# Performance work log

Hardware: AMD Instinct MI355X
Metric: run time of the kernel (lower is better)

The kernel has to match this reference:

```python
import jax, jax.numpy as jnp
import numpy as np

B, N, D, K, CF = 2, 4096, 128, 32, 16
EI = 2 * D + 1  # edge_input_dim = 257 (edge_feat=0, fourier_feat=0)


def setup_inputs() -> dict:
    key = jax.random.key(0)
    ks = jax.random.split(key, 10)
    rn = lambda k, shp, s=0.05: jax.random.normal(k, shp, jnp.float32) * s
    return {
        "h": rn(ks[0], (B, N, D), 1.0),
        "x": rn(ks[1], (B, N, 3), 1.0),
        "mask": jnp.ones((B, N), dtype=bool),
        # edge_mlp: Linear(EI, 2EI) -> SiLU -> Linear(2EI, CF) -> SiLU
        "We1": rn(ks[2], (EI, 2 * EI)), "be1": jnp.zeros((2 * EI,), jnp.float32),
        "We2": rn(ks[3], (2 * EI, CF)), "be2": jnp.zeros((CF,), jnp.float32),
        # coors_mlp: Linear(CF, 4CF) -> SiLU -> Linear(4CF, 1)
        "Wc1": rn(ks[4], (CF, 4 * CF)), "bc1": jnp.zeros((4 * CF,), jnp.float32),
        "Wc2": rn(ks[5], (4 * CF, 1)), "bc2": jnp.zeros((1,), jnp.float32),
        # node_mlp: Linear(D+CF, 2D) -> SiLU -> Linear(2D, D)
        "Wn1": rn(ks[6], (D + CF, 2 * D)), "bn1": jnp.zeros((2 * D,), jnp.float32),
        "Wn2": rn(ks[7], (2 * D, D)), "bn2": jnp.zeros((D,), jnp.float32),
    }


def _forward(h, x, mask, We1, be1, We2, be2, Wc1, bc1, Wc2, bc2, Wn1, bn1, Wn2, bn2):
    silu = jax.nn.silu
    b, n, d = h.shape
    # pairwise relative coordinates and squared distances
    rel = x[:, :, None, :] - x[:, None, :, :]            # [b, n, n, 3]
    dist = jnp.sum(rel * rel, axis=-1)                   # [b, n, n]
    # top-K nearest neighbors (smallest distance)
    _, idx = jax.lax.top_k(-dist, K)                     # [b, n, K]
    rel_k = jnp.take_along_axis(rel, idx[..., None], axis=2)   # [b, n, K, 3]
    dist_k = jnp.take_along_axis(dist, idx, axis=2)[..., None]  # [b, n, K, 1]
    bidx = jnp.arange(b)[:, None, None]
    feats_j = h[bidx, idx]                               # [b, n, K, d]
    feats_i = jnp.broadcast_to(h[:, :, None, :], (b, n, K, d))
    edge_in = jnp.concatenate([feats_i, feats_j, dist_k], axis=-1)  # [b, n, K, 2d+1]
    # edge MLP
    m_ij = silu(silu(edge_in @ We1 + be1) @ We2 + be2)   # [b, n, K, CF]
    # coordinate weights
    cw = (silu(m_ij @ Wc1 + bc1) @ Wc2 + bc2)[..., 0]    # [b, n, K]
    mask_ij = mask[:, :, None] & mask[bidx, idx]         # [b, n, K]
    cw = jnp.where(mask_ij, cw, 0.0)
    coors_out = jnp.einsum('bij,bijc->bic', cw, rel_k) + x
    # node update
    m_i = m_ij.sum(axis=-2)                              # [b, n, CF]
    node_in = jnp.concatenate([h, m_i], axis=-1)
    node_out = silu(node_in @ Wn1 + bn1) @ Wn2 + bn2 + h
    return node_out, coors_out


def reference(h, x, mask, We1, be1, We2, be2, Wc1, bc1, Wc2, bc2, Wn1, bn1, Wn2, bn2):
    return _forward(h, x, mask, We1, be1, We2, be2, Wc1, bc1, Wc2, bc2, Wn1, bn1, Wn2, bn2)
```

## Files before the change

### kernel.cpp

```cpp
#include <hip/hip_runtime.h>
#include <hip/hip_bf16.h>

#define BB    2
#define NNODE 4096
#define DD    128
#define KK    32
#define CFX   16

typedef __attribute__((ext_vector_type(8))) short bf16x8;
typedef __attribute__((ext_vector_type(4))) float f32x4;

__device__ __forceinline__ unsigned short f2bf(float f) {
    __hip_bfloat16 h = __float2bfloat16(f);
    return *reinterpret_cast<unsigned short*>(&h);
}
__device__ __forceinline__ unsigned pk2(float lo, float hi) {
    __hip_bfloat162 v = __float22bfloat162_rn(make_float2(lo, hi));
    return *reinterpret_cast<unsigned*>(&v);
}
__device__ __forceinline__ float silu_f(float v) {
    float e = __expf(-v);
    return v * __builtin_amdgcn_rcpf(1.f + e);
}
__device__ __forceinline__ float dist3(float xi0, float xi1, float xi2,
                                       const float* __restrict__ xb, int j) {
    float d0 = __fsub_rn(xi0, xb[3 * j]);
    float d1 = __fsub_rn(xi1, xb[3 * j + 1]);
    float d2 = __fsub_rn(xi2, xb[3 * j + 2]);
    return __fadd_rn(__fadd_rn(__fmul_rn(d0, d0), __fmul_rn(d1, d1)), __fmul_rn(d2, d2));
}

__global__ void prep_kernel(const float* __restrict__ We1, const float* __restrict__ We2,
                            const float* __restrict__ Wn1, const float* __restrict__ Wn2,
                            unsigned short* __restrict__ W1pack, unsigned short* __restrict__ W2p2,
                            unsigned short* __restrict__ Wn1p, unsigned short* __restrict__ Wn2p) {
    int tid = blockIdx.x * 256 + threadIdx.x;
    int stride = gridDim.x * 256;
    for (int p = tid; p < 9 * 36 * 64 * 8; p += stride) {
        int i = p & 7, lane = (p >> 3) & 63, rest = p >> 9;
        int nb = rest % 36, ks = rest / 36;
        int n = nb * 16 + (lane & 15);
        int k = ks * 32 + 8 * (lane >> 4) + i;
        W1pack[p] = (k < 257 && n < 514) ? f2bf(We1[k * 514 + n]) : (unsigned short)0;
    }
    for (int p = tid; p < 4 * 5 * 64 * 8; p += stride) {
        int i = p & 7, lane = (p >> 3) & 63, rest = p >> 9;
        int ks2 = rest % 5, wn = rest / 5;
        int g = lane >> 4, f = lane & 15;
        int nloc = ks2 * 32 + 16 * (i >> 2) + 4 * g + (i & 3);
        int ng = wn * 144 + nloc;
        W2p2[p] = (nloc < 144 && ng < 514) ? f2bf(We2[ng * 16 + f]) : (unsigned short)0;
    }
    for (int p = tid; p < 5 * 16 * 64 * 8; p += stride) {
        int i = p & 7, lane = (p >> 3) & 63, rest = p >> 9;
        int nb = rest % 16, ks = rest / 16;
        int u = nb * 16 + (lane & 15);
        int k = ks * 32 + 8 * (lane >> 4) + i;
        Wn1p[p] = (k < 144) ? f2bf(Wn1[k * 256 + u]) : (unsigned short)0;
    }
    for (int p = tid; p < 8 * 8 * 64 * 8; p += stride) {
        int i = p & 7, lane = (p >> 3) & 63, rest = p >> 9;
        int nb = rest % 8, ks = rest / 8;
        int d = nb * 16 + (lane & 15);
        int k = ks * 32 + 8 * (lane >> 4) + i;
        Wn2p[p] = f2bf(Wn2[k * 128 + d]);
    }
}

#define EQCAP 36
#define CANDCAP 1024
__global__ __launch_bounds__(256) void knn_kernel(const float* __restrict__ x,
                                                  int* __restrict__ idx_o,
                                                  float* __restrict__ relk_o,
                                                  float* __restrict__ distk_o) {
    __shared__ unsigned hist[4][256];
    __shared__ unsigned wsum[4];
    __shared__ unsigned sel[2];
    __shared__ unsigned shA, shB;
    __shared__ int out_j[KK];
    __shared__ int eqbuf[EQCAP];
    __shared__ uint2 cand[CANDCAP];

    const int t = threadIdx.x;
    const int ln = t & 63, wv = t >> 6;
    const int gn = blockIdx.x;
    const int b = gn >> 12, i = gn & 4095;
    const float* xb = x + (size_t)b * NNODE * 3;
    const float xi0 = xb[3 * i], xi1 = xb[3 * i + 1], xi2 = xb[3 * i + 2];

    #pragma unroll
    for (int q2 = 0; q2 < 4; ++q2) hist[q2][t] = 0;
    __syncthreads();

    unsigned ub[16];
    #pragma unroll
    for (int s = 0; s < 16; ++s) {
        float d = dist3(xi0, xi1, xi2, xb, t + 256 * s);
        ub[s] = __float_as_uint(d);
        atomicAdd(&hist[wv][ub[s] >> 24], 1u);
    }
    __syncthreads();

    int kk = KK;
    {
        unsigned hv = hist[0][t] + hist[1][t] + hist[2][t] + hist[3][t];
        unsigned v = hv;
        #pragma unroll
        for (int off = 1; off < 64; off <<= 1) {
            unsigned o = __shfl_up(v, off, 64);
            if (ln >= off) v += o;
        }
        if (ln == 63) wsum[wv] = v;
        __syncthreads();
        unsigned add = 0;
        #pragma unroll
        for (int w = 0; w < 4; ++w) add += (w < wv) ? wsum[w] : 0u;
        unsigned incl = v + add, excl = incl - hv;
        if ((unsigned)kk > excl && (unsigned)kk <= incl) { sel[0] = (unsigned)t; sel[1] = (unsigned)kk - excl; }
        __syncthreads();
    }
    unsigned prefix = sel[0];
    kk = (int)sel[1];
    __syncthreads();

    unsigned pc = 0;
    #pragma unroll
    for (int s = 0; s < 16; ++s) {
        unsigned tb = ub[s] >> 24;
        pc += (tb < prefix) ? 0x10000u : (tb == prefix ? 1u : 0u);
    }
    {
        unsigned v = pc;
        #pragma unroll
        for (int off = 1; off < 64; off <<= 1) {
            unsigned o = __shfl_up(v, off, 64);
            if (ln >= off) v += o;
        }
        if (ln == 63) wsum[wv] = v;
        __syncthreads();
        unsigned add = 0;
        #pragma unroll
        for (int w = 0; w < 4; ++w) add += (w < wv) ? wsum[w] : 0u;
        unsigned incl = v + add, excl = incl - pc;
        if (t == 255) { shA = incl >> 16; shB = incl & 0xFFFFu; }
        __syncthreads();
        unsigned wl = excl >> 16, wc = excl & 0xFFFFu;
        #pragma unroll
        for (int s = 0; s < 16; ++s) {
            unsigned u = ub[s];
            unsigned tb = u >> 24;
            int j = t + 256 * s;
            if (tb < prefix) { out_j[wl++] = j; }
            else if (tb == prefix) { if (wc < CANDCAP) cand[wc] = make_uint2(u, (unsigned)j); ++wc; }
        }
    }
    __syncthreads();
    const unsigned totL0 = shA, totC = shB;
    const bool fullscan = (totC > CANDCAP);

    for (int r = 1; r < 4; ++r) {
        const int sh = 24 - 8 * r;
        #pragma unroll
        for (int q2 = 0; q2 < 4; ++q2) hist[q2][t] = 0;
        __syncthreads();
        if (!fullscan) {
            for (int ii = t; ii < (int)totC; ii += 256) {
                unsigned u = cand[ii].x;
                if ((u >> (sh + 8)) == prefix) atomicAdd(&hist[wv][(u >> sh) & 255], 1u);
            }
        } else {
            #pragma unroll
            for (int s = 0; s < 16; ++s) {
                unsigned u = ub[s];
                if ((u >> (sh + 8)) == prefix) atomicAdd(&hist[wv][(u >> sh) & 255], 1u);
            }
        }
        __syncthreads();
        unsigned hv = hist[0][t] + hist[1][t] + hist[2][t] + hist[3][t];
        unsigned v = hv;
        #pragma unroll
        for (int off = 1; off < 64; off <<= 1) {
            unsigned o = __shfl_up(v, off, 64);
            if (ln >= off) v += o;
        }
        if (ln == 63) wsum[wv] = v;
        __syncthreads();
        unsigned add = 0;
        #pragma unroll
        for (int w = 0; w < 4; ++w) add += (w < wv) ? wsum[w] : 0u;
        unsigned incl = v + add, excl = incl - hv;
        if ((unsigned)kk > excl && (unsigned)kk <= incl) { sel[0] = (unsigned)t; sel[1] = (unsigned)kk - excl; }
        __syncthreads();
        prefix = (prefix << 8) | sel[0];
        kk = (int)sel[1];
        __syncthreads();
    }
    const unsigned T = prefix;

    int totL;
    if (!fullscan) {
        unsigned pc2 = 0;
        for (int ii = t; ii < (int)totC; ii += 256) {
            unsigned u = cand[ii].x;
            pc2 += (u < T) ? 0x10000u : (u == T ? 1u : 0u);
        }
        unsigned v = pc2;
        #pragma unroll
        for (int off = 1; off < 64; off <<= 1) {
            unsigned o = __shfl_up(v, off, 64);
            if (ln >= off) v += o;
        }
        if (ln == 63) wsum[wv] = v;
        __syncthreads();
        unsigned add = 0;
        #pragma unroll
        for (int w = 0; w < 4; ++w) add += (w < wv) ? wsum[w] : 0u;
        unsigned incl = v + add, excl = incl - pc2;
        if (t == 255) { shA = incl >> 16; shB = incl & 0xFFFFu; }
        __syncthreads();
        unsigned w2 = totL0 + (excl >> 16), we = excl & 0xFFFFu;
        for (int ii = t; ii < (int)totC; ii += 256) {
            unsigned u = cand[ii].x;
            int j = (int)cand[ii].y;
            if (u < T) { out_j[w2++] = j; }
            else if (u == T) { if (we < EQCAP) eqbuf[we] = j; ++we; }
        }
        __syncthreads();
        totL = (int)(totL0 + shA);
        const unsigned totE = shB;
        if (t == 0) {
            int need = KK - totL;
            if (totE <= EQCAP) {
                for (int a = 1; a < (int)totE; ++a) {
                    int key = eqbuf[a], c = a - 1;
                    while (c >= 0 && eqbuf[c] > key) { eqbuf[c + 1] = eqbuf[c]; --c; }
                    eqbuf[c + 1] = key;
                }
                for (int q = 0; q < need; ++q) out_j[totL + q] = eqbuf[q];
            } else {
                int taken = 0;
                for (int j = 0; j < NNODE && taken < need; ++j)
                    if (__float_as_uint(dist3(xi0, xi1, xi2, xb, j)) == T) out_j[totL + taken++] = j;
            }
        }
    } else {
        unsigned pc2 = 0;
        #pragma unroll
        for (int s = 0; s < 16; ++s) {
            unsigned u = ub[s];
            pc2 += (u < T) ? 0x10000u : (u == T ? 1u : 0u);
        }
        unsigned v = pc2;
        #pragma unroll
        for (int off = 1; off < 64; off <<= 1) {
            unsigned o = __shfl_up(v, off, 64);
            if (ln >= off) v += o;
        }
        if (ln == 63) wsum[wv] = v;
        __syncthreads();
        unsigned add = 0;
        #pragma unroll
        for (int w = 0; w < 4; ++w) add += (w < wv) ? wsum[w] : 0u;
        unsigned incl = v + add, excl = incl - pc2;
        if (t == 255) { shA = incl >> 16; shB = incl & 0xFFFFu; }
        __syncthreads();
        unsigned w2 = excl >> 16, we = excl & 0xFFFFu;
        #pragma unroll
        for (int s = 0; s < 16; ++s) {
            unsigned u = ub[s];
            int j = t + 256 * s;
            if (u < T) { out_j[w2++] = j; }
            else if (u == T) { if (we < EQCAP) eqbuf[we] = j; ++we; }
        }
        __syncthreads();
        totL = (int)shA;
        const unsigned totE = shB;
        if (t == 0) {
            int need = KK - totL;
            if (totE <= EQCAP) {
                for (int a = 1; a < (int)totE; ++a) {
                    int key = eqbuf[a], c = a - 1;
                    while (c >= 0 && eqbuf[c] > key) { eqbuf[c + 1] = eqbuf[c]; --c; }
                    eqbuf[c + 1] = key;
                }
                for (int q = 0; q < need; ++q) out_j[totL + q] = eqbuf[q];
            } else {
                int taken = 0;
                for (int j = 0; j < NNODE && taken < need; ++j)
                    if (__float_as_uint(dist3(xi0, xi1, xi2, xb, j)) == T) out_j[totL + taken++] = j;
            }
        }
    }
    __syncthreads();

    if (t < KK) {
        int j = out_j[t];
        size_t eo = (size_t)gn * KK + t;
        idx_o[eo] = j;
        float r0 = __fsub_rn(xi0, xb[3 * j]);
        float r1 = __fsub_rn(xi1, xb[3 * j + 1]);
        float r2 = __fsub_rn(xi2, xb[3 * j + 2]);
        relk_o[eo * 3 + 0] = r0;
        relk_o[eo * 3 + 1] = r1;
        relk_o[eo * 3 + 2] = r2;
        distk_o[eo] = __fadd_rn(__fadd_rn(__fmul_rn(r0, r0), __fmul_rn(r1, r1)), __fmul_rn(r2, r2));
    }
}

__global__ __launch_bounds__(256, 2) void edge_kernel(
    const float* __restrict__ h, const float* __restrict__ x, const int* __restrict__ mask,
    const float* __restrict__ be1, const float* __restrict__ be2,
    const float* __restrict__ Wc1, const float* __restrict__ bc1,
    const float* __restrict__ Wc2, const float* __restrict__ bc2,
    const int* __restrict__ idx, const float* __restrict__ relk, const float* __restrict__ distk,
    const unsigned short* __restrict__ W1pack, const unsigned short* __restrict__ W2p2,
    float* __restrict__ m_i_out, float* __restrict__ coors_out)
{
    __shared__ unsigned short E2[64][168];
    __shared__ unsigned short hi_s[2][136];
    __shared__ float be1s[576];
    __shared__ int   j_s[64];
    __shared__ float cw_s[64];
    __shared__ float m_s4[4 * 64 * 16];
    __shared__ float m_sF[64 * 17];

    const int t = threadIdx.x;
    const int gn0 = blockIdx.x * 2;
    const int b = gn0 >> 12;
    const int wn = t >> 6, lane = t & 63;
    const int l15 = lane & 15, g = lane >> 4;

    if (t < 64) {
        size_t eo = (size_t)gn0 * KK + t;
        j_s[t] = idx[eo];
        float dv = distk[eo];
        ushort2* p = (ushort2*)&E2[t][128];
        p[0] = make_ushort2(f2bf(dv), 0);
        #pragma unroll
        for (int z = 1; z < 20; ++z) p[z] = make_ushort2(0, 0);
    }
    {
        int n = t >> 7, c = t & 127;
        hi_s[n][c] = f2bf(h[(size_t)(gn0 + n) * DD + c]);
    }
    for (int i2 = t; i2 < 576; i2 += 256) be1s[i2] = (i2 < 514) ? be1[i2] : 0.f;
    __syncthreads();

    for (int q = t; q < 64 * 32; q += 256) {
        int e = q >> 5, d4 = q & 31;
        int j = j_s[e];
        float4 v = *(const float4*)(h + ((size_t)b * NNODE + j) * DD + d4 * 4);
        *(uint2*)&E2[e][d4 * 4] = make_uint2(pk2(v.x, v.y), pk2(v.z, v.w));
    }
    __syncthreads();

    const bf16x8* W1v = (const bf16x8*)W1pack;
    const bf16x8* W2v = (const bf16x8*)W2p2;
    int erow[4];
    #pragma unroll
    for (int et = 0; et < 4; ++et) erow[et] = et * 16 + l15;

    f32x4 acc2[4];
    #pragma unroll
    for (int et = 0; et < 4; ++et)
        #pragma unroll
        for (int r = 0; r < 4; ++r) acc2[et][r] = 0.f;

    #pragma unroll
    for (int c = 0; c < 2; ++c) {
        f32x4 acc[4][4];
        #pragma unroll
        for (int nb = 0; nb < 4; ++nb)
            #pragma unroll
            for (int et = 0; et < 4; ++et)
                #pragma unroll
                for (int r = 0; r < 4; ++r) acc[nb][et][r] = 0.f;
        #pragma unroll
        for (int ks = 0; ks < 9; ++ks) {
            const bf16x8* wp = W1v + ((size_t)(ks * 36 + wn * 9 + c * 4)) * 64 + lane;
            bf16x8 afr[4];
            #pragma unroll
            for (int nb = 0; nb < 4; ++nb) afr[nb] = wp[nb * 64];
            bf16x8 bfr[4];
            if (ks < 4) {
                bf16x8 b0 = *(const bf16x8*)&hi_s[0][ks * 32 + 8 * g];
                bf16x8 b1 = *(const bf16x8*)&hi_s[1][ks * 32 + 8 * g];
                bfr[0] = b0; bfr[1] = b0; bfr[2] = b1; bfr[3] = b1;
            } else {
                #pragma unroll
                for (int et = 0; et < 4; ++et)
                    bfr[et] = *(const bf16x8*)&E2[erow[et]][(ks - 4) * 32 + 8 * g];
            }
            #pragma unroll
            for (int nb = 0; nb < 4; ++nb)
                #pragma unroll
                for (int et = 0; et < 4; ++et)
                    acc[nb][et] = __builtin_amdgcn_mfma_f32_16x16x32_bf16(afr[nb], bfr[et], acc[nb][et], 0, 0, 0);
        }
        #pragma unroll
        for (int nb = 0; nb < 4; ++nb) {
            f32x4 bv = *(const f32x4*)&be1s[wn * 144 + (c * 4 + nb) * 16 + 4 * g];
            #pragma unroll
            for (int et = 0; et < 4; ++et)
                #pragma unroll
                for (int r = 0; r < 4; ++r)
                    acc[nb][et][r] = silu_f(acc[nb][et][r] + bv[r]);
        }
        #pragma unroll
        for (int qq = 0; qq < 2; ++qq) {
            int ks2 = 2 * c + qq;
            bf16x8 a2 = W2v[(size_t)(wn * 5 + ks2) * 64 + lane];
            #pragma unroll
            for (int et = 0; et < 4; ++et) {
                union { unsigned u[4]; bf16x8 v; } cv;
                cv.u[0] = pk2(acc[2 * qq][et][0], acc[2 * qq][et][1]);
                cv.u[1] = pk2(acc[2 * qq][et][2], acc[2 * qq][et][3]);
                cv.u[2] = pk2(acc[2 * qq + 1][et][0], acc[2 * qq + 1][et][1]);
                cv.u[3] = pk2(acc[2 * qq + 1][et][2], acc[2 * qq + 1][et][3]);
                acc2[et] = __builtin_amdgcn_mfma_f32_16x16x32_bf16(a2, cv.v, acc2[et], 0, 0, 0);
            }
        }
    }
    {
        f32x4 acc8[4];
        #pragma unroll
        for (int et = 0; et < 4; ++et)
            #pragma unroll
            for (int r = 0; r < 4; ++r) acc8[et][r] = 0.f;
        #pragma unroll
        for (int ks = 0; ks < 9; ++ks) {
            bf16x8 af = W1v[((size_t)(ks * 36 + wn * 9 + 8)) * 64 + lane];
            bf16x8 bfr[4];
            if (ks < 4) {
                bf16x8 b0 = *(const bf16x8*)&hi_s[0][ks * 32 + 8 * g];
                bf16x8 b1 = *(const bf16x8*)&hi_s[1][ks * 32 + 8 * g];
                bfr[0] = b0; bfr[1] = b0; bfr[2] = b1; bfr[3] = b1;
            } else {
                #pragma unroll
                for (int et = 0; et < 4; ++et)
                    bfr[et] = *(const bf16x8*)&E2[erow[et]][(ks - 4) * 32 + 8 * g];
            }
            #pragma unroll
            for (int et = 0; et < 4; ++et)
                acc8[et] = __builtin_amdgcn_mfma_f32_16x16x32_bf16(af, bfr[et], acc8[et], 0, 0, 0);
        }
        f32x4 bv = *(const f32x4*)&be1s[wn * 144 + 128 + 4 * g];
        #pragma unroll
        for (int et = 0; et < 4; ++et)
            #pragma unroll
            for (int r = 0; r < 4; ++r)
                acc8[et][r] = silu_f(acc8[et][r] + bv[r]);
        bf16x8 a2 = W2v[(size_t)(wn * 5 + 4) * 64 + lane];
        #pragma unroll
        for (int et = 0; et < 4; ++et) {
            union { unsigned u[4]; bf16x8 v; } cv;
            cv.u[0] = pk2(acc8[et][0], acc8[et][1]);
            cv.u[1] = pk2(acc8[et][2], acc8[et][3]);
            cv.u[2] = 0; cv.u[3] = 0;
            acc2[et] = __builtin_amdgcn_mfma_f32_16x16x32_bf16(a2, cv.v, acc2[et], 0, 0, 0);
        }
    }
    #pragma unroll
    for (int et = 0; et < 4; ++et)
        *(f32x4*)&m_s4[((wn * 64) + erow[et]) * 16 + 4 * g] = acc2[et];
    __syncthreads();

    #pragma unroll
    for (int i2 = t; i2 < 64 * 16; i2 += 256) {
        int e = i2 >> 4, f = i2 & 15;
        float s = m_s4[e * 16 + f] + m_s4[(64 + e) * 16 + f]
                + m_s4[(128 + e) * 16 + f] + m_s4[(192 + e) * 16 + f];
        m_sF[e * 17 + f] = silu_f(s + be2[f]);
    }
    __syncthreads();

    {
        const int ee = t >> 2, q4 = t & 3;
        const int u0 = q4 * 16;
        float mm[16];
        #pragma unroll
        for (int f = 0; f < 16; ++f) mm[f] = m_sF[ee * 17 + f];
        float h2[16];
        {
            const float4* bp = (const float4*)(bc1 + u0);
            float4 b0 = bp[0], b1 = bp[1], b2v = bp[2], b3 = bp[3];
            h2[0]=b0.x; h2[1]=b0.y; h2[2]=b0.z; h2[3]=b0.w;
            h2[4]=b1.x; h2[5]=b1.y; h2[6]=b1.z; h2[7]=b1.w;
            h2[8]=b2v.x; h2[9]=b2v.y; h2[10]=b2v.z; h2[11]=b2v.w;
            h2[12]=b3.x; h2[13]=b3.y; h2[14]=b3.z; h2[15]=b3.w;
        }
        #pragma unroll
        for (int f = 0; f < 16; ++f) {
            const float4* wp = (const float4*)(Wc1 + (size_t)f * 64 + u0);
            float4 w0 = wp[0], w1 = wp[1], w2 = wp[2], w3 = wp[3];
            float v = mm[f];
            h2[0]  = fmaf(v, w0.x, h2[0]);  h2[1]  = fmaf(v, w0.y, h2[1]);
            h2[2]  = fmaf(v, w0.z, h2[2]);  h2[3]  = fmaf(v, w0.w, h2[3]);
            h2[4]  = fmaf(v, w1.x, h2[4]);  h2[5]  = fmaf(v, w1.y, h2[5]);
            h2[6]  = fmaf(v, w1.z, h2[6]);  h2[7]  = fmaf(v, w1.w, h2[7]);
            h2[8]  = fmaf(v, w2.x, h2[8]);  h2[9]  = fmaf(v, w2.y, h2[9]);
            h2[10] = fmaf(v, w2.z, h2[10]); h2[11] = fmaf(v, w2.w, h2[11]);
            h2[12] = fmaf(v, w3.x, h2[12]); h2[13] = fmaf(v, w3.y, h2[13]);
            h2[14] = fmaf(v, w3.z, h2[14]); h2[15] = fmaf(v, w3.w, h2[15]);
        }
        float cw = 0.f;
        const float4* cp = (const float4*)(Wc2 + u0);
        float4 c0 = cp[0], c1 = cp[1], c2 = cp[2], c3 = cp[3];
        const float wv[16] = {c0.x,c0.y,c0.z,c0.w, c1.x,c1.y,c1.z,c1.w,
                              c2.x,c2.y,c2.z,c2.w, c3.x,c3.y,c3.z,c3.w};
        #pragma unroll
        for (int r = 0; r < 16; ++r) cw = fmaf(silu_f(h2[r]), wv[r], cw);
        cw += __shfl_xor(cw, 1, 64);
        cw += __shfl_xor(cw, 2, 64);
        if (q4 == 0) {
            cw += bc2[0];
            int gnode = gn0 + (ee >> 5);
            int mi = mask[gnode];
            int mj = mask[b * NNODE + j_s[ee]];
            cw_s[ee] = (mi != 0 && mj != 0) ? cw : 0.f;
        }
    }
    __syncthreads();

    if (t < 32) {
        int n = t >> 4, f = t & 15;
        float s = 0.f;
        #pragma unroll
        for (int k2 = 0; k2 < 32; ++k2) s += m_sF[(n * 32 + k2) * 17 + f];
        m_i_out[(size_t)(gn0 + n) * CFX + f] = s;
    } else if (t < 38) {
        int r = t - 32;
        int n = r / 3, c = r - n * 3;
        const float* rp = relk + ((size_t)gn0 * KK + n * 32) * 3 + c;
        float s = 0.f;
        #pragma unroll
        for (int k2 = 0; k2 < 32; ++k2) s = fmaf(cw_s[n * 32 + k2], rp[k2 * 3], s);
        coors_out[(size_t)(gn0 + n) * 3 + c] = s + x[(size_t)(gn0 + n) * 3 + c];
    }
}

__global__ __launch_bounds__(256) void node_kernel(
    const float* __restrict__ h, const float* __restrict__ m_i,
    const unsigned short* __restrict__ Wn1p, const float* __restrict__ bn1,
    const unsigned short* __restrict__ Wn2p, const float* __restrict__ bn2,
    float* __restrict__ node_out)
{
    __shared__ unsigned short nin[32][168];
    __shared__ unsigned short hid[32][264];

    const int t = threadIdx.x;
    const int gn0 = blockIdx.x * 32;
    const int wn = t >> 6, lane = t & 63;
    const int l15 = lane & 15, g = lane >> 4;

    for (int q = t; q < 32 * 32; q += 256) {
        int node = q >> 5, c4 = q & 31;
        float4 v = *(const float4*)(h + (size_t)(gn0 + node) * DD + c4 * 4);
        *(uint2*)&nin[node][c4 * 4] = make_uint2(pk2(v.x, v.y), pk2(v.z, v.w));
    }
    if (t < 128) {
        int node = t >> 2, c4 = t & 3;
        float4 v = *(const float4*)(m_i + (size_t)(gn0 + node) * CFX + c4 * 4);
        *(uint2*)&nin[node][128 + c4 * 4] = make_uint2(pk2(v.x, v.y), pk2(v.z, v.w));
    } else if (t < 224) {
        int r = t - 128;
        int node = r / 3, cc = (r - node * 3) * 8;
        *(uint4*)&nin[node][144 + cc] = make_uint4(0, 0, 0, 0);
    }
    __syncthreads();
// ... 65 lines not shown
            float4 o;
            o.x = acc2[nb][et][0] + bv[0] + hv.x;
            o.y = acc2[nb][et][1] + bv[1] + hv.y;
            o.z = acc2[nb][et][2] + bv[2] + hv.z;
            o.w = acc2[nb][et][3] + bv[3] + hv.w;
            *(float4*)(node_out + (size_t)gnode * DD + d0) = o;
        }
    }
}

extern "C" void kernel_launch(void* const* d_in, const int* in_sizes, int n_in,
                              void* d_out, int out_size, void* d_ws, size_t ws_size,
                              hipStream_t stream) {
    const float* h   = (const float*)d_in[0];
    const float* x   = (const float*)d_in[1];
    const int*   mask= (const int*)d_in[2];
    const float* We1 = (const float*)d_in[3];
    const float* be1 = (const float*)d_in[4];
    const float* We2 = (const float*)d_in[5];
    const float* be2 = (const float*)d_in[6];
    const float* Wc1 = (const float*)d_in[7];
    const float* bc1 = (const float*)d_in[8];
    const float* Wc2 = (const float*)d_in[9];
    const float* bc2 = (const float*)d_in[10];
    const float* Wn1 = (const float*)d_in[11];
    const float* bn1 = (const float*)d_in[12];
    const float* Wn2 = (const float*)d_in[13];
    const float* bn2 = (const float*)d_in[14];

    float* node_out  = (float*)d_out;
    float* coors_out = node_out + (size_t)BB * NNODE * DD;

    char* ws = (char*)d_ws;
    int*   idx    = (int*)ws;            ws += (size_t)BB * NNODE * KK * 4;
    float* relk   = (float*)ws;          ws += (size_t)BB * NNODE * KK * 3 * 4;
    float* distk  = (float*)ws;          ws += (size_t)BB * NNODE * KK * 4;
    float* m_i    = (float*)ws;          ws += (size_t)BB * NNODE * CFX * 4;
    unsigned short* W1pack = (unsigned short*)ws;  ws += (size_t)9 * 36 * 64 * 8 * 2;
    unsigned short* W2p2   = (unsigned short*)ws;  ws += (size_t)4 * 5 * 64 * 8 * 2;
    unsigned short* Wn1p   = (unsigned short*)ws;  ws += (size_t)5 * 16 * 64 * 8 * 2;
    unsigned short* Wn2p   = (unsigned short*)ws;  ws += (size_t)8 * 8 * 64 * 8 * 2;

    prep_kernel<<<256, 256, 0, stream>>>(We1, We2, Wn1, Wn2, W1pack, W2p2, Wn1p, Wn2p);
    knn_kernel<<<BB * NNODE, 256, 0, stream>>>(x, idx, relk, distk);
    edge_kernel<<<BB * NNODE / 2, 256, 0, stream>>>(h, x, mask, be1, be2, Wc1, bc1, Wc2, bc2,
                                                    idx, relk, distk, W1pack, W2p2,
                                                    m_i, coors_out);
    node_kernel<<<BB * NNODE / 32, 256, 0, stream>>>(h, m_i, Wn1p, bn1, Wn2p, bn2, node_out);
}
```

Baseline: 328.7 us.

## Fuse kNN radix-select into edge kernel, removing idx/relk/dist global buffers

```diff
diff --git a/kernel.cpp b/kernel.cpp
--- a/kernel.cpp
+++ b/kernel.cpp
@@ -22,8 +22,8 @@
     float e = __expf(-v);
     return v * __builtin_amdgcn_rcpf(1.f + e);
 }
-__device__ __forceinline__ float dist3(float xi0, float xi1, float xi2,
-                                       const float* __restrict__ xb, int j) {
+__device__ __forceinline__ float dist3c(float xi0, float xi1, float xi2,
+                                        const float* __restrict__ xb, int j) {
     float d0 = __fsub_rn(xi0, xb[3 * j]);
     float d1 = __fsub_rn(xi1, xb[3 * j + 1]);
     float d2 = __fsub_rn(xi2, xb[3 * j + 2]);
@@ -69,250 +69,11 @@
 
 #define EQCAP 36
 #define CANDCAP 1024
-__global__ __launch_bounds__(256) void knn_kernel(const float* __restrict__ x,
-                                                  int* __restrict__ idx_o,
-                                                  float* __restrict__ relk_o,
-                                                  float* __restrict__ distk_o) {
-    __shared__ unsigned hist[4][256];
-    __shared__ unsigned wsum[4];
-    __shared__ unsigned sel[2];
-    __shared__ unsigned shA, shB;
-    __shared__ int out_j[KK];
-    __shared__ int eqbuf[EQCAP];
-    __shared__ uint2 cand[CANDCAP];
-
-    const int t = threadIdx.x;
-    const int ln = t & 63, wv = t >> 6;
-    const int gn = blockIdx.x;
-    const int b = gn >> 12, i = gn & 4095;
-    const float* xb = x + (size_t)b * NNODE * 3;
-    const float xi0 = xb[3 * i], xi1 = xb[3 * i + 1], xi2 = xb[3 * i + 2];
-
-    #pragma unroll
-    for (int q2 = 0; q2 < 4; ++q2) hist[q2][t] = 0;
-    __syncthreads();
-
-    unsigned ub[16];
-    #pragma unroll
-    for (int s = 0; s < 16; ++s) {
-        float d = dist3(xi0, xi1, xi2, xb, t + 256 * s);
-        ub[s] = __float_as_uint(d);
-        atomicAdd(&hist[wv][ub[s] >> 24], 1u);
-    }
-    __syncthreads();
-
-    int kk = KK;
-    {
-        unsigned hv = hist[0][t] + hist[1][t] + hist[2][t] + hist[3][t];
-        unsigned v = hv;
-        #pragma unroll
-        for (int off = 1; off < 64; off <<= 1) {
-            unsigned o = __shfl_up(v, off, 64);
-            if (ln >= off) v += o;
-        }
-        if (ln == 63) wsum[wv] = v;
-        __syncthreads();
-        unsigned add = 0;
-        #pragma unroll
-        for (int w = 0; w < 4; ++w) add += (w < wv) ? wsum[w] : 0u;
-        unsigned incl = v + add, excl = incl - hv;
-        if ((unsigned)kk > excl && (unsigned)kk <= incl) { sel[0] = (unsigned)t; sel[1] = (unsigned)kk - excl; }
-        __syncthreads();
-    }
-    unsigned prefix = sel[0];
-    kk = (int)sel[1];
-    __syncthreads();
-
-    unsigned pc = 0;
-    #pragma unroll
-    for (int s = 0; s < 16; ++s) {
-        unsigned tb = ub[s] >> 24;
-        pc += (tb < prefix) ? 0x10000u : (tb == prefix ? 1u : 0u);
-    }
-    {
-        unsigned v = pc;
-        #pragma unroll
-        for (int off = 1; off < 64; off <<= 1) {
-            unsigned o = __shfl_up(v, off, 64);
-            if (ln >= off) v += o;
-        }
-        if (ln == 63) wsum[wv] = v;
-        __syncthreads();
-        unsigned add = 0;
-        #pragma unroll
-        for (int w = 0; w < 4; ++w) add += (w < wv) ? wsum[w] : 0u;
-        unsigned incl = v + add, excl = incl - pc;
-        if (t == 255) { shA = incl >> 16; shB = incl & 0xFFFFu; }
-        __syncthreads();
-        unsigned wl = excl >> 16, wc = excl & 0xFFFFu;
-        #pragma unroll
-        for (int s = 0; s < 16; ++s) {
-            unsigned u = ub[s];
-            unsigned tb = u >> 24;
-            int j = t + 256 * s;
-            if (tb < prefix) { out_j[wl++] = j; }
-            else if (tb == prefix) { if (wc < CANDCAP) cand[wc] = make_uint2(u, (unsigned)j); ++wc; }
-        }
-    }
-    __syncthreads();
-    const unsigned totL0 = shA, totC = shB;
-    const bool fullscan = (totC > CANDCAP);
-
-    for (int r = 1; r < 4; ++r) {
-        const int sh = 24 - 8 * r;
-        #pragma unroll
-        for (int q2 = 0; q2 < 4; ++q2) hist[q2][t] = 0;
-        __syncthreads();
-        if (!fullscan) {
-            for (int ii = t; ii < (int)totC; ii += 256) {
-                unsigned u = cand[ii].x;
-                if ((u >> (sh + 8)) == prefix) atomicAdd(&hist[wv][(u >> sh) & 255], 1u);
-            }
-        } else {
-            #pragma unroll
-            for (int s = 0; s < 16; ++s) {
-                unsigned u = ub[s];
-                if ((u >> (sh + 8)) == prefix) atomicAdd(&hist[wv][(u >> sh) & 255], 1u);
-            }
-        }
-        __syncthreads();
-        unsigned hv = hist[0][t] + hist[1][t] + hist[2][t] + hist[3][t];
-        unsigned v = hv;
-        #pragma unroll
-        for (int off = 1; off < 64; off <<= 1) {
-            unsigned o = __shfl_up(v, off, 64);
-            if (ln >= off) v += o;
-        }
-        if (ln == 63) wsum[wv] = v;
-        __syncthreads();
-        unsigned add = 0;
-        #pragma unroll
-        for (int w = 0; w < 4; ++w) add += (w < wv) ? wsum[w] : 0u;
-        unsigned incl = v + add, excl = incl - hv;
-        if ((unsigned)kk > excl && (unsigned)kk <= incl) { sel[0] = (unsigned)t; sel[1] = (unsigned)kk - excl; }
-        __syncthreads();
-        prefix = (prefix << 8) | sel[0];
-        kk = (int)sel[1];
-        __syncthreads();
-    }
-    const unsigned T = prefix;
-
-    int totL;
-    if (!fullscan) {
-        unsigned pc2 = 0;
-        for (int ii = t; ii < (int)totC; ii += 256) {
-            unsigned u = cand[ii].x;
-            pc2 += (u < T) ? 0x10000u : (u == T ? 1u : 0u);
-        }
-        unsigned v = pc2;
-        #pragma unroll
-        for (int off = 1; off < 64; off <<= 1) {
-            unsigned o = __shfl_up(v, off, 64);
-            if (ln >= off) v += o;
-        }
-        if (ln == 63) wsum[wv] = v;
-        __syncthreads();
-        unsigned add = 0;
-        #pragma unroll
-        for (int w = 0; w < 4; ++w) add += (w < wv) ? wsum[w] : 0u;
-        unsigned incl = v + add, excl = incl - pc2;
-        if (t == 255) { shA = incl >> 16; shB = incl & 0xFFFFu; }
-        __syncthreads();
-        unsigned w2 = totL0 + (excl >> 16), we = excl & 0xFFFFu;
-        for (int ii = t; ii < (int)totC; ii += 256) {
-            unsigned u = cand[ii].x;
-            int j = (int)cand[ii].y;
-            if (u < T) { out_j[w2++] = j; }
-            else if (u == T) { if (we < EQCAP) eqbuf[we] = j; ++we; }
-        }
-        __syncthreads();
-        totL = (int)(totL0 + shA);
-        const unsigned totE = shB;
-        if (t == 0) {
-            int need = KK - totL;
-            if (totE <= EQCAP) {
-                for (int a = 1; a < (int)totE; ++a) {
-                    int key = eqbuf[a], c = a - 1;
-                    while (c >= 0 && eqbuf[c] > key) { eqbuf[c + 1] = eqbuf[c]; --c; }
-                    eqbuf[c + 1] = key;
-                }
-                for (int q = 0; q < need; ++q) out_j[totL + q] = eqbuf[q];
-            } else {
-                int taken = 0;
-                for (int j = 0; j < NNODE && taken < need; ++j)
-                    if (__float_as_uint(dist3(xi0, xi1, xi2, xb, j)) == T) out_j[totL + taken++] = j;
-            }
-        }
-    } else {
-        unsigned pc2 = 0;
-        #pragma unroll
-        for (int s = 0; s < 16; ++s) {
-            unsigned u = ub[s];
-            pc2 += (u < T) ? 0x10000u : (u == T ? 1u : 0u);
-        }
-        unsigned v = pc2;
-        #pragma unroll
-        for (int off = 1; off < 64; off <<= 1) {
-            unsigned o = __shfl_up(v, off, 64);
-            if (ln >= off) v += o;
-        }
-        if (ln == 63) wsum[wv] = v;
-        __syncthreads();
-        unsigned add = 0;
-        #pragma unroll
-        for (int w = 0; w < 4; ++w) add += (w < wv) ? wsum[w] : 0u;
-        unsigned incl = v + add, excl = incl - pc2;
-        if (t == 255) { shA = incl >> 16; shB = incl & 0xFFFFu; }
-        __syncthreads();
-        unsigned w2 = excl >> 16, we = excl & 0xFFFFu;
-        #pragma unroll
-        for (int s = 0; s < 16; ++s) {
-            unsigned u = ub[s];
-            int j = t + 256 * s;
-            if (u < T) { out_j[w2++] = j; }
-            else if (u == T) { if (we < EQCAP) eqbuf[we] = j; ++we; }
-        }
-        __syncthreads();
-        totL = (int)shA;
-        const unsigned totE = shB;
-        if (t == 0) {
-            int need = KK - totL;
-            if (totE <= EQCAP) {
-                for (int a = 1; a < (int)totE; ++a) {
-                    int key = eqbuf[a], c = a - 1;
-                    while (c >= 0 && eqbuf[c] > key) { eqbuf[c + 1] = eqbuf[c]; --c; }
-                    eqbuf[c + 1] = key;
-                }
-                for (int q = 0; q < need; ++q) out_j[totL + q] = eqbuf[q];
-            } else {
-                int taken = 0;
-                for (int j = 0; j < NNODE && taken < need; ++j)
-                    if (__float_as_uint(dist3(xi0, xi1, xi2, xb, j)) == T) out_j[totL + taken++] = j;
-            }
-        }
-    }
-    __syncthreads();
-
-    if (t < KK) {
-        int j = out_j[t];
-        size_t eo = (size_t)gn * KK + t;
-        idx_o[eo] = j;
-        float r0 = __fsub_rn(xi0, xb[3 * j]);
-        float r1 = __fsub_rn(xi1, xb[3 * j + 1]);
-        float r2 = __fsub_rn(xi2, xb[3 * j + 2]);
-        relk_o[eo * 3 + 0] = r0;
-        relk_o[eo * 3 + 1] = r1;
-        relk_o[eo * 3 + 2] = r2;
-        distk_o[eo] = __fadd_rn(__fadd_rn(__fmul_rn(r0, r0), __fmul_rn(r1, r1)), __fmul_rn(r2, r2));
-    }
-}
-
 __global__ __launch_bounds__(256, 2) void edge_kernel(
     const float* __restrict__ h, const float* __restrict__ x, const int* __restrict__ mask,
     const float* __restrict__ be1, const float* __restrict__ be2,
     const float* __restrict__ Wc1, const float* __restrict__ bc1,
     const float* __restrict__ Wc2, const float* __restrict__ bc2,
-    const int* __restrict__ idx, const float* __restrict__ relk, const float* __restrict__ distk,
     const unsigned short* __restrict__ W1pack, const unsigned short* __restrict__ W2p2,
     float* __restrict__ m_i_out, float* __restrict__ coors_out)
 {
@@ -323,29 +84,279 @@
     __shared__ float cw_s[64];
     __shared__ float m_s4[4 * 64 * 16];
     __shared__ float m_sF[64 * 17];
+    __shared__ float dist_e[64];
+    __shared__ float rel_s[64][3];
 
     const int t = threadIdx.x;
     const int gn0 = blockIdx.x * 2;
     const int b = gn0 >> 12;
     const int wn = t >> 6, lane = t & 63;
     const int l15 = lane & 15, g = lane >> 4;
-
-    if (t < 64) {
-        size_t eo = (size_t)gn0 * KK + t;
-        j_s[t] = idx[eo];
-        float dv = distk[eo];
-        ushort2* p = (ushort2*)&E2[t][128];
-        p[0] = make_ushort2(f2bf(dv), 0);
-        #pragma unroll
-        for (int z = 1; z < 20; ++z) p[z] = make_ushort2(0, 0);
-    }
+    const int ln = lane, wv = wn;
+
     {
         int n = t >> 7, c = t & 127;
         hi_s[n][c] = f2bf(h[(size_t)(gn0 + n) * DD + c]);
     }
     for (int i2 = t; i2 < 576; i2 += 256) be1s[i2] = (i2 < 514) ? be1[i2] : 0.f;
+
+    {
+        unsigned* histA = (unsigned*)m_s4;
+        uint2*    candA = (uint2*)(m_s4 + 2048);
+        unsigned* wsum  = (unsigned*)m_sF;
+        unsigned* sel   = wsum + 4;
+        unsigned* shAB  = sel + 2;
+        int* out_jA     = (int*)(shAB + 2);
+        int* eqbufA     = out_jA + 32;
+
+        const float* xb = x + (size_t)b * NNODE * 3;
+        const int i0 = gn0 & 4095;
+        float xi[2][3];
+        #pragma unroll
+        for (int q = 0; q < 2; ++q) {
+            xi[q][0] = xb[3 * (i0 + q)];
+            xi[q][1] = xb[3 * (i0 + q) + 1];
+            xi[q][2] = xb[3 * (i0 + q) + 2];
+        }
+        for (int z = t; z < 2048; z += 256) histA[z] = 0;
+        __syncthreads();
+
+        unsigned ub[2][16];
+        #pragma unroll
+        for (int s = 0; s < 16; ++s) {
+            int j = t + 256 * s;
+            float xj0 = xb[3 * j], xj1 = xb[3 * j + 1], xj2 = xb[3 * j + 2];
+            #pragma unroll
+            for (int q = 0; q < 2; ++q) {
+                float d0 = __fsub_rn(xi[q][0], xj0);
+                float d1 = __fsub_rn(xi[q][1], xj1);
+                float d2 = __fsub_rn(xi[q][2], xj2);
+                float d = __fadd_rn(__fadd_rn(__fmul_rn(d0, d0), __fmul_rn(d1, d1)), __fmul_rn(d2, d2));
+                ub[q][s] = __float_as_uint(d);
+                atomicAdd(&histA[(q * 4 + wv) * 256 + (ub[q][s] >> 24)], 1u);
+            }
+        }
+        __syncthreads();
+
+        #pragma unroll
+        for (int q = 0; q < 2; ++q) {
+            int kk = KK;
+            {
+                unsigned hv = histA[(q * 4 + 0) * 256 + t] + histA[(q * 4 + 1) * 256 + t]
+                            + histA[(q * 4 + 2) * 256 + t] + histA[(q * 4 + 3) * 256 + t];
+                unsigned v = hv;
+                #pragma unroll
+                for (int off = 1; off < 64; off <<= 1) {
+                    unsigned o = __shfl_up(v, off, 64);
+                    if (ln >= off) v += o;
+                }
+                if (ln == 63) wsum[wv] = v;
+                __syncthreads();
+                unsigned add = 0;
+                #pragma unroll
+                for (int w = 0; w < 4; ++w) add += (w < wv) ? wsum[w] : 0u;
+                unsigned incl = v + add, excl = incl - hv;
+                if ((unsigned)kk > excl && (unsigned)kk <= incl) { sel[0] = (unsigned)t; sel[1] = (unsigned)kk - excl; }
+                __syncthreads();
+            }
+            unsigned prefix = sel[0];
+            kk = (int)sel[1];
+            __syncthreads();
+
+            unsigned pc = 0;
+            #pragma unroll
+            for (int s = 0; s < 16; ++s) {
+                unsigned tb = ub[q][s] >> 24;
+                pc += (tb < prefix) ? 0x10000u : (tb == prefix ? 1u : 0u);
+            }
+            {
+                unsigned v = pc;
+                #pragma unroll
+                for (int off = 1; off < 64; off <<= 1) {
+                    unsigned o = __shfl_up(v, off, 64);
+                    if (ln >= off) v += o;
+                }
+                if (ln == 63) wsum[wv] = v;
+                __syncthreads();
+                unsigned add = 0;
+                #pragma unroll
+                for (int w = 0; w < 4; ++w) add += (w < wv) ? wsum[w] : 0u;
+                unsigned incl = v + add, excl = incl - pc;
+                if (t == 255) { shAB[0] = incl >> 16; shAB[1] = incl & 0xFFFFu; }
+                __syncthreads();
+                unsigned wl = excl >> 16, wc = excl & 0xFFFFu;
+                #pragma unroll
+                for (int s = 0; s < 16; ++s) {
+                    unsigned u = ub[q][s];
+                    unsigned tb = u >> 24;
+                    int j = t + 256 * s;
+                    if (tb < prefix) { out_jA[wl++] = j; }
+                    else if (tb == prefix) { if (wc < CANDCAP) candA[wc] = make_uint2(u, (unsigned)j); ++wc; }
+                }
+            }
+            __syncthreads();
+            const unsigned totL0 = shAB[0], totC = shAB[1];
+            const bool fullscan = (totC > CANDCAP);
+
+            for (int r = 1; r < 4; ++r) {
+                const int sh = 24 - 8 * r;
+                #pragma unroll
+                for (int q2 = 0; q2 < 4; ++q2) histA[q2 * 256 + t] = 0;
+                __syncthreads();
+                if (!fullscan) {
+                    for (int ii = t; ii < (int)totC; ii += 256) {
+                        unsigned u = candA[ii].x;
+                        if ((u >> (sh + 8)) == prefix) atomicAdd(&histA[wv * 256 + ((u >> sh) & 255)], 1u);
+                    }
+                } else {
+                    #pragma unroll
+                    for (int s = 0; s < 16; ++s) {
+                        unsigned u = ub[q][s];
+                        if ((u >> (sh + 8)) == prefix) atomicAdd(&histA[wv * 256 + ((u >> sh) & 255)], 1u);
+                    }
+                }
+                __syncthreads();
+                unsigned hv = histA[t] + histA[256 + t] + histA[512 + t] + histA[768 + t];
+                unsigned v = hv;
+                #pragma unroll
+                for (int off = 1; off < 64; off <<= 1) {
+                    unsigned o = __shfl_up(v, off, 64);
+                    if (ln >= off) v += o;
+                }
+                if (ln == 63) wsum[wv] = v;
+                __syncthreads();
+                unsigned add = 0;
+                #pragma unroll
+                for (int w = 0; w < 4; ++w) add += (w < wv) ? wsum[w] : 0u;
+                unsigned incl = v + add, excl = incl - hv;
+                if ((unsigned)kk > excl && (unsigned)kk <= incl) { sel[0] = (unsigned)t; sel[1] = (unsigned)kk - excl; }
+                __syncthreads();
+                prefix = (prefix << 8) | sel[0];
+                kk = (int)sel[1];
+                __syncthreads();
+            }
+            const unsigned T = prefix;
+
+            int totL;
+            if (!fullscan) {
+                unsigned pc2 = 0;
+                for (int ii = t; ii < (int)totC; ii += 256) {
+                    unsigned u = candA[ii].x;
+                    pc2 += (u < T) ? 0x10000u : (u == T ? 1u : 0u);
+                }
+                unsigned v = pc2;
+                #pragma unroll
+                for (int off = 1; off < 64; off <<= 1) {
+                    unsigned o = __shfl_up(v, off, 64);
+                    if (ln >= off) v += o;
+                }
+                if (ln == 63) wsum[wv] = v;
+                __syncthreads();
+                unsigned add = 0;
+                #pragma unroll
+                for (int w = 0; w < 4; ++w) add += (w < wv) ? wsum[w] : 0u;
+                unsigned incl = v + add, excl = incl - pc2;
+                if (t == 255) { shAB[0] = incl >> 16; shAB[1] = incl & 0xFFFFu; }
+                __syncthreads();
+                unsigned w2 = totL0 + (excl >> 16), we = excl & 0xFFFFu;
+                for (int ii = t; ii < (int)totC; ii += 256) {
+                    unsigned u = candA[ii].x;
+                    int j = (int)candA[ii].y;
+                    if (u < T) { out_jA[w2++] = j; }
+                    else if (u == T) { if (we < EQCAP) eqbufA[we] = j; ++we; }
+                }
+                __syncthreads();
+                totL = (int)(totL0 + shAB[0]);
+                const unsigned totE = shAB[1];
+                if (t == 0) {
+                    int need = KK - totL;
+                    if (totE <= EQCAP) {
+                        for (int a = 1; a < (int)totE; ++a) {
+                            int key = eqbufA[a], c = a - 1;
+                            while (c >= 0 && eqbufA[c] > key) { eqbufA[c + 1] = eqbufA[c]; --c; }
+                            eqbufA[c + 1] = key;
+                        }
+                        for (int q3 = 0; q3 < need; ++q3) out_jA[totL + q3] = eqbufA[q3];
+                    } else {
+                        int taken = 0;
+                        for (int j = 0; j < NNODE && taken < need; ++j)
+                            if (__float_as_uint(dist3c(xi[q][0], xi[q][1], xi[q][2], xb, j)) == T)
+                                out_jA[totL + taken++] = j;
+                    }
+                }
+            } else {
+                unsigned pc2 = 0;
+                #pragma unroll
+                for (int s = 0; s < 16; ++s) {
+                    unsigned u = ub[q][s];
+                    pc2 += (u < T) ? 0x10000u : (u == T ? 1u : 0u);
+                }
+                unsigned v = pc2;
+                #pragma unroll
+                for (int off = 1; off < 64; off <<= 1) {
+                    unsigned o = __shfl_up(v, off, 64);
+                    if (ln >= off) v += o;
+                }
+                if (ln == 63) wsum[wv] = v;
+                __syncthreads();
+                unsigned add = 0;
+                #pragma unroll
+                for (int w = 0; w < 4; ++w) add += (w < wv) ? wsum[w] : 0u;
+                unsigned incl = v + add, excl = incl - pc2;
+                if (t == 255) { shAB[0] = incl >> 16; shAB[1] = incl & 0xFFFFu; }
+                __syncthreads();
+                unsigned w2 = excl >> 16, we = excl & 0xFFFFu;
+                #pragma unroll
+                for (int s = 0; s < 16; ++s) {
+                    unsigned u = ub[q][s];
+                    int j = t + 256 * s;
+                    if (u < T) { out_jA[w2++] = j; }
+                    else if (u == T) { if (we < EQCAP) eqbufA[we] = j; ++we; }
+                }
+                __syncthreads();
+                totL = (int)shAB[0];
+                const unsigned totE = shAB[1];
+                if (t == 0) {
+                    int need = KK - totL;
+                    if (totE <= EQCAP) {
+                        for (int a = 1; a < (int)totE; ++a) {
+                            int key = eqbufA[a], c = a - 1;
+                            while (c >= 0 && eqbufA[c] > key) { eqbufA[c + 1] = eqbufA[c]; --c; }
+                            eqbufA[c + 1] = key;
+                        }
+                        for (int q3 = 0; q3 < need; ++q3) out_jA[totL + q3] = eqbufA[q3];
+                    } else {
+                        int taken = 0;
+                        for (int j = 0; j < NNODE && taken < need; ++j)
+                            if (__float_as_uint(dist3c(xi[q][0], xi[q][1], xi[q][2], xb, j)) == T)
+                                out_jA[totL + taken++] = j;
+                    }
+                }
+            }
+            __syncthreads();
+
+            if (t < KK) {
+                int j = out_jA[t];
+                int e = q * 32 + t;
+                j_s[e] = j;
+                float r0 = __fsub_rn(xi[q][0], xb[3 * j]);
+                float r1 = __fsub_rn(xi[q][1], xb[3 * j + 1]);
+                float r2 = __fsub_rn(xi[q][2], xb[3 * j + 2]);
+                rel_s[e][0] = r0;
+                rel_s[e][1] = r1;
+                rel_s[e][2] = r2;
+                dist_e[e] = __fadd_rn(__fadd_rn(__fmul_rn(r0, r0), __fmul_rn(r1, r1)), __fmul_rn(r2, r2));
+            }
+            __syncthreads();
+        }
+    }
+    if (t < 64) {
+        ushort2* p = (ushort2*)&E2[t][128];
+        p[0] = make_ushort2(f2bf(dist_e[t]), 0);
+        #pragma unroll
+        for (int z = 1; z < 20; ++z) p[z] = make_ushort2(0, 0);
+    }
     __syncthreads();
-
     for (int q = t; q < 64 * 32; q += 256) {
         int e = q >> 5, d4 = q & 31;
         int j = j_s[e];
@@ -506,10 +517,10 @@
         float cw = 0.f;
         const float4* cp = (const float4*)(Wc2 + u0);
         float4 c0 = cp[0], c1 = cp[1], c2 = cp[2], c3 = cp[3];
-        const float wv[16] = {c0.x,c0.y,c0.z,c0.w, c1.x,c1.y,c1.z,c1.w,
-                              c2.x,c2.y,c2.z,c2.w, c3.x,c3.y,c3.z,c3.w};
-        #pragma unroll
-        for (int r = 0; r < 16; ++r) cw = fmaf(silu_f(h2[r]), wv[r], cw);
+        const float wv2[16] = {c0.x,c0.y,c0.z,c0.w, c1.x,c1.y,c1.z,c1.w,
+                               c2.x,c2.y,c2.z,c2.w, c3.x,c3.y,c3.z,c3.w};
+        #pragma unroll
+        for (int r = 0; r < 16; ++r) cw = fmaf(silu_f(h2[r]), wv2[r], cw);
         cw += __shfl_xor(cw, 1, 64);
         cw += __shfl_xor(cw, 2, 64);
         if (q4 == 0) {
@@ -531,10 +542,9 @@
     } else if (t < 38) {
         int r = t - 32;
         int n = r / 3, c = r - n * 3;
-        const float* rp = relk + ((size_t)gn0 * KK + n * 32) * 3 + c;
         float s = 0.f;
         #pragma unroll
-        for (int k2 = 0; k2 < 32; ++k2) s = fmaf(cw_s[n * 32 + k2], rp[k2 * 3], s);
+        for (int k2 = 0; k2 < 32; ++k2) s = fmaf(cw_s[n * 32 + k2], rel_s[n * 32 + k2][c], s);
         coors_out[(size_t)(gn0 + n) * 3 + c] = s + x[(size_t)(gn0 + n) * 3 + c];
     }
 }
@@ -666,9 +676,6 @@
     float* coors_out = node_out + (size_t)BB * NNODE * DD;
 
     char* ws = (char*)d_ws;
-    int*   idx    = (int*)ws;            ws += (size_t)BB * NNODE * KK * 4;
-    float* relk   = (float*)ws;          ws += (size_t)BB * NNODE * KK * 3 * 4;
-    float* distk  = (float*)ws;          ws += (size_t)BB * NNODE * KK * 4;
     float* m_i    = (float*)ws;          ws += (size_t)BB * NNODE * CFX * 4;
     unsigned short* W1pack = (unsigned short*)ws;  ws += (size_t)9 * 36 * 64 * 8 * 2;
     unsigned short* W2p2   = (unsigned short*)ws;  ws += (size_t)4 * 5 * 64 * 8 * 2;
@@ -676,9 +683,7 @@
     unsigned short* Wn2p   = (unsigned short*)ws;  ws += (size_t)8 * 8 * 64 * 8 * 2;
 
     prep_kernel<<<256, 256, 0, stream>>>(We1, We2, Wn1, Wn2, W1pack, W2p2, Wn1p, Wn2p);
-    knn_kernel<<<BB * NNODE, 256, 0, stream>>>(x, idx, relk, distk);
     edge_kernel<<<BB * NNODE / 2, 256, 0, stream>>>(h, x, mask, be1, be2, Wc1, bc1, Wc2, bc2,
-                                                    idx, relk, distk, W1pack, W2p2,
-                                                    m_i, coors_out);
+                                                    W1pack, W2p2, m_i, coors_out);
     node_kernel<<<BB * NNODE / 32, 256, 0, stream>>>(h, m_i, Wn1p, bn1, Wn2p, bn2, node_out);
 }
```

After: 360.7 us. 1.1x slower.

## Precompute per-node h_i·We1 term once instead of per edge

Applied to the files above, without the earlier changes.

```diff
diff --git a/kernel.cpp b/kernel.cpp
--- a/kernel.cpp
+++ b/kernel.cpp
@@ -64,6 +64,51 @@
         int d = nb * 16 + (lane & 15);
         int k = ks * 32 + 8 * (lane >> 4) + i;
         Wn2p[p] = f2bf(Wn2[k * 128 + d]);
+    }
+}
+
+__global__ __launch_bounds__(256) void pre_kernel(
+    const float* __restrict__ h, const float* __restrict__ be1,
+    const unsigned short* __restrict__ W1pack, float* __restrict__ pre_g)
+{
+    __shared__ unsigned short nin[16][136];
+    const int t = threadIdx.x;
+    const int gn0 = blockIdx.x * 16;
+    const int wn = t >> 6, lane = t & 63;
+    const int l15 = lane & 15, g = lane >> 4;
+
+    for (int q = t; q < 16 * 32; q += 256) {
+        int node = q >> 5, c4 = q & 31;
+        float4 v = *(const float4*)(h + (size_t)(gn0 + node) * DD + c4 * 4);
+        *(uint2*)&nin[node][c4 * 4] = make_uint2(pk2(v.x, v.y), pk2(v.z, v.w));
+    }
+    __syncthreads();
+
+    const bf16x8* W1v = (const bf16x8*)W1pack;
+    f32x4 acc[9];
+    #pragma unroll
+    for (int nb = 0; nb < 9; ++nb)
+        #pragma unroll
+        for (int r = 0; r < 4; ++r) acc[nb][r] = 0.f;
+    #pragma unroll
+    for (int ks = 0; ks < 4; ++ks) {
+        bf16x8 bfr = *(const bf16x8*)&nin[l15][ks * 32 + 8 * g];
+        #pragma unroll
+        for (int nb = 0; nb < 9; ++nb) {
+            bf16x8 af = W1v[((size_t)(ks * 36 + wn * 9 + nb)) * 64 + lane];
+            acc[nb] = __builtin_amdgcn_mfma_f32_16x16x32_bf16(af, bfr, acc[nb], 0, 0, 0);
+        }
+    }
+    float* outp = pre_g + (size_t)(gn0 + l15) * 576;
+    #pragma unroll
+    for (int nb = 0; nb < 9; ++nb) {
+        int n0 = wn * 144 + nb * 16 + 4 * g;
+        float4 o;
+        o.x = acc[nb][0] + ((n0 + 0) < 514 ? be1[n0 + 0] : 0.f);
+        o.y = acc[nb][1] + ((n0 + 1) < 514 ? be1[n0 + 1] : 0.f);
+        o.z = acc[nb][2] + ((n0 + 2) < 514 ? be1[n0 + 2] : 0.f);
+        o.w = acc[nb][3] + ((n0 + 3) < 514 ? be1[n0 + 3] : 0.f);
+        *(float4*)(outp + n0) = o;
     }
 }
 
@@ -309,16 +354,16 @@
 
 __global__ __launch_bounds__(256, 2) void edge_kernel(
     const float* __restrict__ h, const float* __restrict__ x, const int* __restrict__ mask,
-    const float* __restrict__ be1, const float* __restrict__ be2,
+    const float* __restrict__ be2,
     const float* __restrict__ Wc1, const float* __restrict__ bc1,
     const float* __restrict__ Wc2, const float* __restrict__ bc2,
     const int* __restrict__ idx, const float* __restrict__ relk, const float* __restrict__ distk,
     const unsigned short* __restrict__ W1pack, const unsigned short* __restrict__ W2p2,
+    const float* __restrict__ pre_g,
     float* __restrict__ m_i_out, float* __restrict__ coors_out)
 {
     __shared__ unsigned short E2[64][168];
-    __shared__ unsigned short hi_s[2][136];
-    __shared__ float be1s[576];
+    __shared__ float pre_s[2 * 576];
     __shared__ int   j_s[64];
     __shared__ float cw_s[64];
     __shared__ float m_s4[4 * 64 * 16];
@@ -340,10 +385,10 @@
         for (int z = 1; z < 20; ++z) p[z] = make_ushort2(0, 0);
     }
     {
-        int n = t >> 7, c = t & 127;
-        hi_s[n][c] = f2bf(h[(size_t)(gn0 + n) * DD + c]);
-    }
-    for (int i2 = t; i2 < 576; i2 += 256) be1s[i2] = (i2 < 514) ? be1[i2] : 0.f;
+        const float4* src = (const float4*)(pre_g + (size_t)gn0 * 576);
+        float4* dst = (float4*)pre_s;
+        for (int i2 = t; i2 < 288; i2 += 256) dst[i2] = src[i2];
+    }
     __syncthreads();
 
     for (int q = t; q < 64 * 32; q += 256) {
@@ -373,24 +418,17 @@
         for (int nb = 0; nb < 4; ++nb)
             #pragma unroll
             for (int et = 0; et < 4; ++et)
-                #pragma unroll
-                for (int r = 0; r < 4; ++r) acc[nb][et][r] = 0.f;
-        #pragma unroll
-        for (int ks = 0; ks < 9; ++ks) {
-            const bf16x8* wp = W1v + ((size_t)(ks * 36 + wn * 9 + c * 4)) * 64 + lane;
+                acc[nb][et] = *(const f32x4*)&pre_s[(et >> 1) * 576 + wn * 144 + (c * 4 + nb) * 16 + 4 * g];
+        #pragma unroll
+        for (int ks = 0; ks < 5; ++ks) {
+            const bf16x8* wp = W1v + ((size_t)((ks + 4) * 36 + wn * 9 + c * 4)) * 64 + lane;
             bf16x8 afr[4];
             #pragma unroll
             for (int nb = 0; nb < 4; ++nb) afr[nb] = wp[nb * 64];
             bf16x8 bfr[4];
-            if (ks < 4) {
-                bf16x8 b0 = *(const bf16x8*)&hi_s[0][ks * 32 + 8 * g];
-                bf16x8 b1 = *(const bf16x8*)&hi_s[1][ks * 32 + 8 * g];
-                bfr[0] = b0; bfr[1] = b0; bfr[2] = b1; bfr[3] = b1;
-            } else {
-                #pragma unroll
-                for (int et = 0; et < 4; ++et)
-                    bfr[et] = *(const bf16x8*)&E2[erow[et]][(ks - 4) * 32 + 8 * g];
-            }
+            #pragma unroll
+            for (int et = 0; et < 4; ++et)
+                bfr[et] = *(const bf16x8*)&E2[erow[et]][ks * 32 + 8 * g];
             #pragma unroll
             for (int nb = 0; nb < 4; ++nb)
                 #pragma unroll
@@ -398,14 +436,12 @@
                     acc[nb][et] = __builtin_amdgcn_mfma_f32_16x16x32_bf16(afr[nb], bfr[et], acc[nb][et], 0, 0, 0);
         }
         #pragma unroll
-        for (int nb = 0; nb < 4; ++nb) {
-            f32x4 bv = *(const f32x4*)&be1s[wn * 144 + (c * 4 + nb) * 16 + 4 * g];
+        for (int nb = 0; nb < 4; ++nb)
             #pragma unroll
             for (int et = 0; et < 4; ++et)
                 #pragma unroll
                 for (int r = 0; r < 4; ++r)
-                    acc[nb][et][r] = silu_f(acc[nb][et][r] + bv[r]);
-        }
+                    acc[nb][et][r] = silu_f(acc[nb][et][r]);
         #pragma unroll
         for (int qq = 0; qq < 2; ++qq) {
             int ks2 = 2 * c + qq;
@@ -425,31 +461,23 @@
         f32x4 acc8[4];
         #pragma unroll
         for (int et = 0; et < 4; ++et)
-            #pragma unroll
-            for (int r = 0; r < 4; ++r) acc8[et][r] = 0.f;
-        #pragma unroll
-        for (int ks = 0; ks < 9; ++ks) {
-            bf16x8 af = W1v[((size_t)(ks * 36 + wn * 9 + 8)) * 64 + lane];
+            acc8[et] = *(const f32x4*)&pre_s[(et >> 1) * 576 + wn * 144 + 128 + 4 * g];
+        #pragma unroll
+        for (int ks = 0; ks < 5; ++ks) {
+            bf16x8 af = W1v[((size_t)((ks + 4) * 36 + wn * 9 + 8)) * 64 + lane];
             bf16x8 bfr[4];
-            if (ks < 4) {
-                bf16x8 b0 = *(const bf16x8*)&hi_s[0][ks * 32 + 8 * g];
-                bf16x8 b1 = *(const bf16x8*)&hi_s[1][ks * 32 + 8 * g];
-                bfr[0] = b0; bfr[1] = b0; bfr[2] = b1; bfr[3] = b1;
-            } else {
-                #pragma unroll
-                for (int et = 0; et < 4; ++et)
-                    bfr[et] = *(const bf16x8*)&E2[erow[et]][(ks - 4) * 32 + 8 * g];
-            }
+            #pragma unroll
+            for (int et = 0; et < 4; ++et)
+                bfr[et] = *(const bf16x8*)&E2[erow[et]][ks * 32 + 8 * g];
             #pragma unroll
             for (int et = 0; et < 4; ++et)
                 acc8[et] = __builtin_amdgcn_mfma_f32_16x16x32_bf16(af, bfr[et], acc8[et], 0, 0, 0);
         }
-        f32x4 bv = *(const f32x4*)&be1s[wn * 144 + 128 + 4 * g];
         #pragma unroll
         for (int et = 0; et < 4; ++et)
             #pragma unroll
             for (int r = 0; r < 4; ++r)
-                acc8[et][r] = silu_f(acc8[et][r] + bv[r]);
+                acc8[et][r] = silu_f(acc8[et][r]);
         bf16x8 a2 = W2v[(size_t)(wn * 5 + 4) * 64 + lane];
         #pragma unroll
         for (int et = 0; et < 4; ++et) {
@@ -674,11 +702,13 @@
     unsigned short* W2p2   = (unsigned short*)ws;  ws += (size_t)4 * 5 * 64 * 8 * 2;
     unsigned short* Wn1p   = (unsigned short*)ws;  ws += (size_t)5 * 16 * 64 * 8 * 2;
     unsigned short* Wn2p   = (unsigned short*)ws;  ws += (size_t)8 * 8 * 64 * 8 * 2;
+    float* pre_g  = (float*)ws;          ws += (size_t)BB * NNODE * 576 * 4;
 
     prep_kernel<<<256, 256, 0, stream>>>(We1, We2, Wn1, Wn2, W1pack, W2p2, Wn1p, Wn2p);
+    pre_kernel<<<BB * NNODE / 16, 256, 0, stream>>>(h, be1, W1pack, pre_g);
     knn_kernel<<<BB * NNODE, 256, 0, stream>>>(x, idx, relk, distk);
-    edge_kernel<<<BB * NNODE / 2, 256, 0, stream>>>(h, x, mask, be1, be2, Wc1, bc1, Wc2, bc2,
-                                                    idx, relk, distk, W1pack, W2p2,
+    edge_kernel<<<BB * NNODE / 2, 256, 0, stream>>>(h, x, mask, be2, Wc1, bc1, Wc2, bc2,
+                                                    idx, relk, distk, W1pack, W2p2, pre_g,
                                                     m_i, coors_out);
     node_kernel<<<BB * NNODE / 32, 256, 0, stream>>>(h, m_i, Wn1p, bn1, Wn2p, bn2, node_out);
 }
```

Result: faster. 288.0 us (-12.4%).
